# Kernel optimization log

Hardware: AMD Instinct MI355X
Metric: run time of the kernel (lower is better)

## Reference

```python
import jax, jax.numpy as jnp
import numpy as np

INNER = 256   # inner_channel
NODES = 64    # nodes_num (prototypes)
EM_NUM = 3
DIAG_C = 128  # hardcoded diag_channel in FullyConnectGCLayer


def setup_inputs() -> dict:
    key = jax.random.key(0)
    ks = jax.random.split(key, 16)
    b, c, w, h = 4, 1024, 64, 64
    f32 = jnp.float32
    d = {}
    d["x"] = jax.random.normal(ks[0], (b, c, w, h), f32)
    # Conv2d weights re-initialized to N(0, 0.001) in Intra_graph.__init__
    d["W_in"] = 0.001 * jax.random.normal(ks[1], (INNER, c), f32)
    d["b_in"] = jnp.zeros((INNER,), f32)
    d["multi_proto"] = 0.001 * jax.random.normal(ks[2], (1, INNER, NODES), f32)
    d["pi0"] = jnp.ones((1, NODES), f32) / NODES
    # Conv1d layers keep default kaiming-uniform-ish init
    lim = 1.0 / np.sqrt(INNER)
    d["W_adj"] = jax.random.uniform(ks[3], (DIAG_C, INNER), f32, -lim, lim)
    d["b_adj"] = jax.random.uniform(ks[4], (DIAG_C,), f32, -lim, lim)
    d["W_diag"] = jax.random.uniform(ks[5], (DIAG_C, INNER), f32, -lim, lim)
    d["b_diag"] = jax.random.uniform(ks[6], (DIAG_C,), f32, -lim, lim)
    d["gcn_weight"] = 0.01 * jax.random.normal(ks[7], (INNER, INNER), f32)
    d["W_out"] = 0.001 * jax.random.normal(ks[8], (c, INNER), f32)
    d["b_out"] = jnp.zeros((c,), f32)
    d["gamma"] = jnp.ones((c,), f32)
    d["beta"] = jnp.zeros((c,), f32)
    d["W_out2"] = 0.001 * jax.random.normal(ks[9], (c, INNER), f32)
    d["b_out2"] = jnp.zeros((c,), f32)
    d["gamma2"] = jnp.ones((c,), f32)
    d["beta2"] = jnp.zeros((c,), f32)
    d["flag"] = 0
    return d


def _bn(y, g, bt):
    # BatchNorm2d in training mode: batch stats over (N,H,W), biased var, eps=1e-5
    m = jnp.mean(y, (0, 2, 3), keepdims=True)
    v = jnp.var(y, (0, 2, 3), keepdims=True)
    return (y - m) * jax.lax.rsqrt(v + 1e-5) * g[None, :, None, None] + bt[None, :, None, None]


def _forward(x, W_in, b_in, multi_proto, pi0, W_adj, b_adj, W_diag, b_diag,
             gcn_weight, W_out, b_out, gamma, beta, W_out2, b_out2, gamma2, beta2):
    b, c, w, h = x.shape
    wh = w * h
    x1 = (jnp.einsum('oi,bihw->bohw', W_in, x) + b_in[None, :, None, None]).reshape(b, INNER, wh)
    # ---- EM soft-clustering loop (runs under no_grad in torch) ----
    x1s = jax.lax.stop_gradient(x1)
    mu = jnp.broadcast_to(multi_proto, (b, INNER, NODES))
    pi = jnp.broadcast_to(pi0[None, :, :], (b, 1, NODES))
    for _ in range(EM_NUM):
        lik = jnp.einsum('bcm,bcn->bmn', x1s, mu)              # [b, wh, n]
        lik = jnp.exp(lik - jnp.max(lik, 2, keepdims=True))
        post = lik * pi
        post = post / (1e-18 + jnp.sum(post, 2, keepdims=True))
        prob = post / (1e-18 + jnp.sum(post, 1, keepdims=True))
        mu = jnp.einsum('bcm,bmn->bcn', x1s, prob)
        pi = jnp.sum(post, 1, keepdims=True) / wh
    post = jax.lax.stop_gradient(post)
    prob = jax.lax.stop_gradient(prob)
    # ---- aggregate to prototypes (grad flows through x1 only) ----
    x2 = jnp.einsum('bcm,bmn->bcn', x1, prob)                   # [b, inner, n]
    # ---- branch 2: scatter back, conv, bn ----
    x4 = jnp.einsum('bcn,bmn->bcm', x2, post).reshape(b, INNER, w, h)
    x4 = _bn(jnp.einsum('oi,bihw->bohw', W_out2, x4) + b_out2[None, :, None, None], gamma2, beta2)
    output2 = jax.nn.relu(jax.nn.relu(x4) + x)
    # ---- FullyConnectGCLayer on x2 ----
    xd = jnp.einsum('oi,bin->bon', W_diag, x2) + b_diag[None, :, None]
    dvec = jax.nn.sigmoid(jnp.mean(xd, 2))                      # [b, 128]
    xa = jnp.einsum('oi,bin->bon', W_adj, x2) + b_adj[None, :, None]  # [b, 128, n]
    # sigmoid(diag(d)) has 0.5 off-diagonal, sigmoid(d) on diagonal:
    # xa^T S xa = 0.5 * (1^T xa)^T (1^T xa) + xa^T diag(sig(d)-0.5) xa
    u = jnp.sum(xa, 1)                                          # [b, n]
    A = 0.5 * u[:, :, None] * u[:, None, :] + jnp.einsum('bcn,bc,bcm->bnm', xa, dvec - 0.5, xa)
    A = jax.nn.relu(A) + jnp.eye(NODES, dtype=x.dtype)[None]
    deg = jax.lax.stop_gradient(jnp.sum(A, 1) ** -0.5)          # no_grad degree, [b, n]
    A = deg[:, :, None] * A * deg[:, None, :]
    gout = jnp.einsum('oi,bin->bon', gcn_weight, jnp.einsum('bcn,bnm->bcm', x2, A))
    x2g = jax.nn.relu(gout) + x2                                # res_connect
    # ---- branch 1: scatter back, conv, bn ----
    x3 = jnp.einsum('bcn,bmn->bcm', x2g, post).reshape(b, INNER, w, h)
    x3 = _bn(jnp.einsum('oi,bihw->bohw', W_out, x3) + b_out[None, :, None, None], gamma, beta)
    output = jax.nn.relu(jax.nn.relu(x3) + x)
    return output, output2


def reference(x, W_in, b_in, multi_proto, pi0, W_adj, b_adj, W_diag, b_diag,
              gcn_weight, W_out, b_out, gamma, beta, W_out2, b_out2, gamma2, beta2, flag):
    # flag only gates a buffer EMA update (no effect on forward outputs)
    return _forward(x, W_in, b_in, multi_proto, pi0, W_adj, b_adj, W_diag, b_diag,
                    gcn_weight, W_out, b_out, gamma, beta, W_out2, b_out2, gamma2, beta2)
```

## Files before the change

### kernel.cpp

```cpp
#include <hip/hip_runtime.h>
#include <math.h>


typedef unsigned short u16;
typedef short s16x8 __attribute__((ext_vector_type(8)));
typedef float f32x4 __attribute__((ext_vector_type(4)));

constexpr int BB  = 4;
constexpr int CH  = 1024;
constexpr int IN  = 256;
constexpr int ND  = 64;
constexpr int WH  = 4096;
constexpr int DCN = 128;
constexpr size_t TOT = (size_t)BB * CH * WH;

__device__ inline u16 f2bf(float f) {
  unsigned u = __float_as_uint(f);
  return (u16)((u + 0x7fffu + ((u >> 16) & 1u)) >> 16);
}
__device__ inline s16x8 ld8(const u16* p) { return *(const s16x8*)p; }
#define MFMA16(a, b, c) __builtin_amdgcn_mfma_f32_16x16x32_bf16(a, b, c, 0, 0, 0)

__global__ void k_init(const float* __restrict__ Win, const float* __restrict__ mp,
                       const float* __restrict__ pi0, u16* __restrict__ Winb,
                       u16* __restrict__ mu_t, float* __restrict__ piw,
                       float* __restrict__ sp) {
  int idx = blockIdx.x * 256 + threadIdx.x;
  if (idx < IN * CH) { Winb[idx] = f2bf(Win[idx]); return; }
  int j = idx - IN * CH;
  if (j < BB * ND * IN) {
    int bb = j >> 14, n = (j >> 8) & 63, c = j & 255;
    mu_t[((size_t)(bb * ND + n)) * IN + c] = f2bf(mp[c * ND + n]);
    return;
  }
  j -= BB * ND * IN;
  if (j < BB * ND) { piw[j] = pi0[j & 63]; return; }
  j -= BB * ND;
  if (j < 3 * BB * ND) sp[j] = 0.f;
}

__global__ __launch_bounds__(512) void k_x1(
    const float* __restrict__ x, const u16* __restrict__ Winb,
    const float* __restrict__ bin, u16* __restrict__ x1, u16* __restrict__ x1t) {
  __shared__ u16 lt[64][40];
  const int t = threadIdx.x, w = t >> 6, lr = t & 15, lg = (t >> 4) & 3;
  const int wc = w & 3, wm = w >> 2;
  const int m0 = blockIdx.x * 64, b = blockIdx.y;
  const int si = t >> 4, sm = (t & 15) * 4;
  const float* xb = x + (size_t)b * CH * WH + m0 + sm;
  f32x4 acc[4][2];
#pragma unroll
  for (int i = 0; i < 4; ++i)
#pragma unroll
    for (int j = 0; j < 2; ++j) acc[i][j] = (f32x4){0.f, 0.f, 0.f, 0.f};
  const u16* wp = Winb + (size_t)(wc * 64 + lr) * CH + lg * 8;

  float4 nxt = *(const float4*)&xb[(size_t)si * WH];
  for (int k0 = 0; k0 < CH; k0 += 32) {
    float4 cur = nxt;
    __syncthreads();
    lt[sm + 0][si] = f2bf(cur.x); lt[sm + 1][si] = f2bf(cur.y);
    lt[sm + 2][si] = f2bf(cur.z); lt[sm + 3][si] = f2bf(cur.w);
    if (k0 + 32 < CH) nxt = *(const float4*)&xb[(size_t)(k0 + 32 + si) * WH];
    __syncthreads();
    s16x8 af[4], bf[2];
#pragma unroll
    for (int i = 0; i < 4; ++i) af[i] = ld8(wp + (size_t)i * 16 * CH + k0);
#pragma unroll
    for (int j = 0; j < 2; ++j) bf[j] = *(const s16x8*)&lt[wm * 32 + j * 16 + lr][lg * 8];
#pragma unroll
    for (int i = 0; i < 4; ++i)
#pragma unroll
      for (int j = 0; j < 2; ++j) acc[i][j] = MFMA16(af[i], bf[j], acc[i][j]);
  }
#pragma unroll
  for (int i = 0; i < 4; ++i) {
    const int cb = wc * 64 + i * 16 + lg * 4;
    const float4 bi = *(const float4*)&bin[cb];
    const float bia[4] = {bi.x, bi.y, bi.z, bi.w};
#pragma unroll
    for (int j = 0; j < 2; ++j) {
      const int m = m0 + wm * 32 + j * 16 + lr;
      float v[4];
#pragma unroll
      for (int r = 0; r < 4; ++r) v[r] = acc[i][j][r] + bia[r];
      ushort4 o;
      o.x = f2bf(v[0]); o.y = f2bf(v[1]); o.z = f2bf(v[2]); o.w = f2bf(v[3]);
      *(ushort4*)&x1t[((size_t)b * WH + m) * IN + cb] = o;
#pragma unroll
      for (int r = 0; r < 4; ++r)
        x1[((size_t)b * IN + cb + r) * WH + m] = f2bf(v[r]);
    }
  }
}

__global__ __launch_bounds__(256) void k_em(
    const u16* __restrict__ x1, const u16* __restrict__ x1t,
    const u16* __restrict__ mu_t, const float* __restrict__ piw,
    float* __restrict__ sp, u16* __restrict__ pmn,
    float* __restrict__ mup, float* __restrict__ gp, int doG) {
  __shared__ u16 ptl[64][72];
  const int t = threadIdx.x, w = t >> 6, lr = t & 15, lg = (t >> 4) & 3;
  const int mch = blockIdx.x, b = blockIdx.y;
  {
    f32x4 acc[4];
#pragma unroll
    for (int f = 0; f < 4; ++f) acc[f] = (f32x4){0.f, 0.f, 0.f, 0.f};
    const u16* ap = x1t + ((size_t)b * WH + mch * 64 + w * 16 + lr) * IN + lg * 8;
    const u16* bp = mu_t + ((size_t)b * ND + lr) * IN + lg * 8;
#pragma unroll
    for (int k0 = 0; k0 < IN; k0 += 32) {
      s16x8 a = ld8(ap + k0);
#pragma unroll
      for (int f = 0; f < 4; ++f)
        acc[f] = MFMA16(a, ld8(bp + f * 16 * IN + k0), acc[f]);
    }
    float pi_[4], spart[4] = {0.f, 0.f, 0.f, 0.f};
#pragma unroll
    for (int f = 0; f < 4; ++f) pi_[f] = piw[b * ND + f * 16 + lr];
#pragma unroll
    for (int r = 0; r < 4; ++r) {
      float v0 = acc[0][r], v1 = acc[1][r], v2 = acc[2][r], v3 = acc[3][r];
      float mx = fmaxf(fmaxf(v0, v1), fmaxf(v2, v3));
      mx = fmaxf(mx, __shfl_xor(mx, 1)); mx = fmaxf(mx, __shfl_xor(mx, 2));
      mx = fmaxf(mx, __shfl_xor(mx, 4)); mx = fmaxf(mx, __shfl_xor(mx, 8));
      float e0 = __expf(v0 - mx) * pi_[0], e1 = __expf(v1 - mx) * pi_[1];
      float e2 = __expf(v2 - mx) * pi_[2], e3 = __expf(v3 - mx) * pi_[3];
      float s = e0 + e1 + e2 + e3;
      s += __shfl_xor(s, 1); s += __shfl_xor(s, 2);
      s += __shfl_xor(s, 4); s += __shfl_xor(s, 8);
      const float inv = 1.f / (1e-18f + s);
      e0 *= inv; e1 *= inv; e2 *= inv; e3 *= inv;
      const int mloc = w * 16 + lg * 4 + r;
      const size_t gbase = ((size_t)b * WH + mch * 64 + mloc) * ND + lr;
      u16 q0 = f2bf(e0), q1 = f2bf(e1), q2 = f2bf(e2), q3 = f2bf(e3);
      pmn[gbase + 0]  = q0; pmn[gbase + 16] = q1;
      pmn[gbase + 32] = q2; pmn[gbase + 48] = q3;
      ptl[0 + lr][mloc]  = q0; ptl[16 + lr][mloc] = q1;
      ptl[32 + lr][mloc] = q2; ptl[48 + lr][mloc] = q3;
      spart[0] += e0; spart[1] += e1; spart[2] += e2; spart[3] += e3;
    }
#pragma unroll
    for (int f = 0; f < 4; ++f) {
      spart[f] += __shfl_xor(spart[f], 16);
      spart[f] += __shfl_xor(spart[f], 32);
    }
    if (((t >> 4) & 3) == 0) {
#pragma unroll
      for (int f = 0; f < 4; ++f)
        atomicAdd(&sp[b * ND + f * 16 + lr], spart[f]);
    }
  }
  __syncthreads();
  {
    f32x4 acc[4][4];
#pragma unroll
    for (int i = 0; i < 4; ++i)
#pragma unroll
      for (int j = 0; j < 4; ++j) acc[i][j] = (f32x4){0.f, 0.f, 0.f, 0.f};
    const u16* ap = x1 + ((size_t)b * IN + w * 64 + lr) * WH + mch * 64 + lg * 8;
#pragma unroll
    for (int ks = 0; ks < 2; ++ks) {
      s16x8 af[4], bf[4];
#pragma unroll
      for (int i = 0; i < 4; ++i) af[i] = ld8(ap + (size_t)i * 16 * WH + ks * 32);
#pragma unroll
      for (int j = 0; j < 4; ++j)
        bf[j] = *(const s16x8*)&ptl[j * 16 + lr][ks * 32 + lg * 8];
#pragma unroll
      for (int i = 0; i < 4; ++i)
#pragma unroll
        for (int j = 0; j < 4; ++j) acc[i][j] = MFMA16(af[i], bf[j], acc[i][j]);
    }
    float* mo = mup + ((size_t)mch * BB + b) * (IN * ND);
#pragma unroll
    for (int i = 0; i < 4; ++i)
#pragma unroll
      for (int j = 0; j < 4; ++j)
#pragma unroll
        for (int r = 0; r < 4; ++r) {
          const int c = w * 64 + i * 16 + lg * 4 + r, n = j * 16 + lr;
          mo[c * ND + n] = acc[i][j][r];
        }
  }
  if (doG) {
    f32x4 acc[4];
#pragma unroll
    for (int j = 0; j < 4; ++j) acc[j] = (f32x4){0.f, 0.f, 0.f, 0.f};
#pragma unroll
    for (int ks = 0; ks < 2; ++ks) {
      s16x8 a = *(const s16x8*)&ptl[w * 16 + lr][ks * 32 + lg * 8];
#pragma unroll
      for (int j = 0; j < 4; ++j) {
        s16x8 bq = *(const s16x8*)&ptl[j * 16 + lr][ks * 32 + lg * 8];
        acc[j] = MFMA16(a, bq, acc[j]);
      }
    }
    float* go = gp + ((size_t)mch * BB + b) * (ND * ND);
#pragma unroll
    for (int j = 0; j < 4; ++j)
#pragma unroll
      for (int r = 0; r < 4; ++r) {
        const int n1 = w * 16 + lg * 4 + r, n2 = j * 16 + lr;
        go[n1 * ND + n2] = acc[j][r];
      }
  }
}

__global__ void k_mu_red(const float* __restrict__ mup, const float* __restrict__ spb,
                         float* __restrict__ piw, float* __restrict__ mu,
                         u16* __restrict__ mu_t, const float* __restrict__ gp,
                         float* __restrict__ G, int doG) {
  const int idx = blockIdx.x * 256 + threadIdx.x;
  const int bb = idx >> 14, c = (idx >> 6) & 255, n = idx & 63;
  float s = 0.f;
#pragma unroll 8
  for (int ch = 0; ch < 64; ++ch)
    s += mup[((size_t)ch * BB + bb) * (IN * ND) + (idx & 16383)];
  const float v = s / (1e-18f + spb[bb * ND + n]);
  mu[idx] = v;
  mu_t[((size_t)(bb * ND + n)) * IN + c] = f2bf(v);
  if (idx < BB * ND) piw[idx] = spb[idx] * (1.f / (float)WH);
  if (doG && idx < BB * ND * ND) {
    float g = 0.f;
#pragma unroll 8
    for (int ch = 0; ch < 64; ++ch) g += gp[(size_t)ch * (BB * ND * ND) + idx];
    G[idx] = g;
  }
}

__global__ __launch_bounds__(256) void k_gcA(
    const float* __restrict__ mu, const float* __restrict__ gw,
    const float* __restrict__ Wa, const float* __restrict__ ba,
    const float* __restrict__ Wd, const float* __restrict__ bd,
    float* __restrict__ qbuf, float* __restrict__ xabuf, float* __restrict__ dv) {
  __shared__ float sx2[IN * ND];
  __shared__ float srm[IN];
  const int t = threadIdx.x, blk = blockIdx.x, b = blockIdx.y;
  if (blk < 6) {
    const float* src = mu + (size_t)b * IN * ND;
#pragma unroll
    for (int q4 = 0; q4 < 16; ++q4)
      *(float4*)&sx2[q4 * 1024 + t * 4] = *(const float4*)&src[q4 * 1024 + t * 4];
    __syncthreads();
    const int rg = t >> 4, cg = t & 15;
    const float* W = (blk < 4) ? gw + (size_t)(blk * 64 + rg * 4) * IN
                               : Wa + (size_t)((blk - 4) * 64 + rg * 4) * IN;
    float acc[4][4] = {};
    for (int i4 = 0; i4 < 64; ++i4) {
      float4 xv[4];
#pragma unroll
      for (int e = 0; e < 4; ++e)
        xv[e] = *(const float4*)&sx2[(i4 * 4 + e) * 64 + cg * 4];
#pragma unroll
      for (int rr = 0; rr < 4; ++rr) {
        const float4 w4 = *(const float4*)&W[(size_t)rr * IN + i4 * 4];
        acc[rr][0] += w4.x * xv[0].x + w4.y * xv[1].x + w4.z * xv[2].x + w4.w * xv[3].x;
        acc[rr][1] += w4.x * xv[0].y + w4.y * xv[1].y + w4.z * xv[2].y + w4.w * xv[3].y;
        acc[rr][2] += w4.x * xv[0].z + w4.y * xv[1].z + w4.z * xv[2].z + w4.w * xv[3].z;
        acc[rr][3] += w4.x * xv[0].w + w4.y * xv[1].w + w4.z * xv[2].w + w4.w * xv[3].w;
      }
    }
    if (blk < 4) {
      float* dst = qbuf + (size_t)b * IN * ND + (size_t)(blk * 64 + rg * 4) * ND + cg * 4;
#pragma unroll
      for (int rr = 0; rr < 4; ++rr)
        *(float4*)&dst[(size_t)rr * ND] =
            make_float4(acc[rr][0], acc[rr][1], acc[rr][2], acc[rr][3]);
    } else {
      const int xr = (blk - 4) * 64 + rg * 4;
      float* dst = xabuf + (size_t)b * DCN * ND + (size_t)xr * ND + cg * 4;
#pragma unroll
      for (int rr = 0; rr < 4; ++rr) {
        const float bv = ba[xr + rr];
        *(float4*)&dst[(size_t)rr * ND] =
            make_float4(acc[rr][0] + bv, acc[rr][1] + bv, acc[rr][2] + bv, acc[rr][3] + bv);
      }
    }
  } else {
    {
      const float* row = mu + (size_t)b * IN * ND + (size_t)t * ND;
      float s = 0.f;
#pragma unroll
      for (int n4 = 0; n4 < 16; ++n4) {
        float4 v = *(const float4*)&row[n4 * 4];
        s += v.x + v.y + v.z + v.w;
      }
      srm[t] = s * (1.f / ND);
    }
    __syncthreads();
    if (t < DCN) {
      float a = 0.f;
#pragma unroll
      for (int i4 = 0; i4 < 64; ++i4) {
        float4 w4 = *(const float4*)&Wd[(size_t)t * IN + i4 * 4];
        float4 r4 = *(const float4*)&srm[i4 * 4];
        a += w4.x * r4.x + w4.y * r4.y + w4.z * r4.z + w4.w * r4.w;
      }
      a += bd[t];
      dv[b * DCN + t] = 1.f / (1.f + __expf(-a)) - 0.5f;
    }
  }
}

__global__ __launch_bounds__(256) void k_gcB(
    const float* __restrict__ xabuf, const float* __restrict__ dv,
    float* __restrict__ ahat) {
  __shared__ float sxa[DCN * ND];
  __shared__ float sdv[DCN];
  __shared__ float su[ND];
  __shared__ float sdeg[ND];
  __shared__ float sA[ND * 65];
  const int t = threadIdx.x, b = blockIdx.x;
  const float* src = xabuf + (size_t)b * DCN * ND;
#pragma unroll
  for (int q4 = 0; q4 < 8; ++q4)
    *(float4*)&sxa[q4 * 1024 + t * 4] = *(const float4*)&src[q4 * 1024 + t * 4];
  if (t < DCN) sdv[t] = dv[b * DCN + t];
  __syncthreads();
  if (t < ND) {
    float s = 0.f;
    for (int dc = 0; dc < DCN; ++dc) s += sxa[dc * ND + t];
    su[t] = s;
  }
  __syncthreads();
  {
    const int n1g = t >> 4, n2g = t & 15;
    float acc[4][4] = {};
    for (int dc = 0; dc < DCN; ++dc) {
      const float dvv = sdv[dc];
      float4 v1 = *(const float4*)&sxa[dc * ND + n1g * 4];
      const float4 v2 = *(const float4*)&sxa[dc * ND + n2g * 4];
      v1.x *= dvv; v1.y *= dvv; v1.z *= dvv; v1.w *= dvv;
      acc[0][0] += v1.x * v2.x; acc[0][1] += v1.x * v2.y;
      acc[0][2] += v1.x * v2.z; acc[0][3] += v1.x * v2.w;
      acc[1][0] += v1.y * v2.x; acc[1][1] += v1.y * v2.y;
      acc[1][2] += v1.y * v2.z; acc[1][3] += v1.y * v2.w;
      acc[2][0] += v1.z * v2.x; acc[2][1] += v1.z * v2.y;
      acc[2][2] += v1.z * v2.z; acc[2][3] += v1.z * v2.w;
      acc[3][0] += v1.w * v2.x; acc[3][1] += v1.w * v2.y;
      acc[3][2] += v1.w * v2.z; acc[3][3] += v1.w * v2.w;
    }
#pragma unroll
    for (int i = 0; i < 4; ++i) {
      const int n1 = n1g * 4 + i;
      const float u1 = su[n1];
#pragma unroll
      for (int j = 0; j < 4; ++j) {
        const int n2 = n2g * 4 + j;
        const float v = acc[i][j] + 0.5f * u1 * su[n2];
        sA[n1 * 65 + n2] = fmaxf(v, 0.f) + (n1 == n2 ? 1.f : 0.f);
      }
    }
  }
  __syncthreads();
  if (t < ND) {
    float s = 0.f;
    for (int m = 0; m < ND; ++m) s += sA[m * 65 + t];
    sdeg[t] = rsqrtf(s);
  }
  __syncthreads();
  {
    const int n1g = t >> 4, n2g = t & 15;
#pragma unroll
    for (int i = 0; i < 4; ++i) {
      const int n1 = n1g * 4 + i;
      const float dr = sdeg[n1];
      float4 o;
      o.x = dr * sA[n1 * 65 + n2g * 4 + 0] * sdeg[n2g * 4 + 0];
      o.y = dr * sA[n1 * 65 + n2g * 4 + 1] * sdeg[n2g * 4 + 1];
      o.z = dr * sA[n1 * 65 + n2g * 4 + 2] * sdeg[n2g * 4 + 2];
      o.w = dr * sA[n1 * 65 + n2g * 4 + 3] * sdeg[n2g * 4 + 3];
      *(float4*)&ahat[(size_t)b * ND * ND + n1 * ND + n2g * 4] = o;
    }
  }
}

__global__ __launch_bounds__(256) void k_gcC(
    const float* __restrict__ qbuf, const float* __restrict__ ahat,
    const float* __restrict__ mu, float* __restrict__ x2g) {
  __shared__ float sq[64 * 68];
  __shared__ float sAh[64 * 65];
  const int t = threadIdx.x, ro = blockIdx.x * 64, b = blockIdx.y;
  {
    const int r = t >> 2, seg = (t & 3) * 16;
    const float* qs = qbuf + (size_t)b * IN * ND + (size_t)(ro + r) * ND + seg;
#pragma unroll
    for (int f = 0; f < 4; ++f) {
      float4 v = *(const float4*)&qs[f * 4];
      sq[r * 68 + seg + f * 4 + 0] = v.x; sq[r * 68 + seg + f * 4 + 1] = v.y;
      sq[r * 68 + seg + f * 4 + 2] = v.z; sq[r * 68 + seg + f * 4 + 3] = v.w;
    }
    const float* as = ahat + (size_t)b * ND * ND + (size_t)r * ND + seg;
#pragma unroll
    for (int f = 0; f < 4; ++f) {
      float4 v = *(const float4*)&as[f * 4];
      sAh[r * 65 + seg + f * 4 + 0] = v.x; sAh[r * 65 + seg + f * 4 + 1] = v.y;
      sAh[r * 65 + seg + f * 4 + 2] = v.z; sAh[r * 65 + seg + f * 4 + 3] = v.w;
    }
  }
  __syncthreads();
  const int rg = t >> 4, cg = t & 15;
  float acc[4][4] = {};
  for (int k = 0; k < ND; ++k) {
    const float4 a4 = *(const float4*)&sAh[k * 65 + cg * 4];
    float qv[4];
#pragma unroll
    for (int rr = 0; rr < 4; ++rr) qv[rr] = sq[(rg * 4 + rr) * 68 + k];
#pragma unroll
    for (int rr = 0; rr < 4; ++rr) {
      acc[rr][0] += qv[rr] * a4.x; acc[rr][1] += qv[rr] * a4.y;
      acc[rr][2] += qv[rr] * a4.z; acc[rr][3] += qv[rr] * a4.w;
    }
  }
#pragma unroll
  for (int rr = 0; rr < 4; ++rr) {
    const size_t off = (size_t)b * IN * ND + (size_t)(ro + rg * 4 + rr) * ND + cg * 4;
    const float4 xv = *(const float4*)&mu[off];
    float4 o;
    o.x = fmaxf(acc[rr][0], 0.f) + xv.x; o.y = fmaxf(acc[rr][1], 0.f) + xv.y;
    o.z = fmaxf(acc[rr][2], 0.f) + xv.z; o.w = fmaxf(acc[rr][3], 0.f) + xv.w;
    *(float4*)&x2g[off] = o;
  }
}

__global__ __launch_bounds__(256) void k_zdual(
    const float* __restrict__ Wo, const float* __restrict__ v1,
    float* __restrict__ z1o, u16* __restrict__ zb1o,
    const float* __restrict__ Wo2, const float* __restrict__ v2,
    float* __restrict__ z2o, u16* __restrict__ zb2o) {
  const float* W = blockIdx.z ? Wo2 : Wo;
  const float* v = blockIdx.z ? v2 : v1;
  float* z  = blockIdx.z ? z2o : z1o;
  u16* zb   = blockIdx.z ? zb2o : zb1o;
  __shared__ float As[16][68];
  __shared__ float Bs[16][64];
  const int t = threadIdx.x, tx = t & 15, ty = t >> 4;
  const int o0 = blockIdx.x * 64, bb = blockIdx.y;
  const int aoo = t >> 2, akq = (t & 3) * 4;
  const int bkk = t >> 4, bnq = (t & 15) * 4;
  float acc[4][4] = {};
  for (int k0 = 0; k0 < IN; k0 += 16) {
    {
      float4 w4 = *(const float4*)&W[(size_t)(o0 + aoo) * IN + k0 + akq];
      As[akq + 0][aoo] = w4.x; As[akq + 1][aoo] = w4.y;
      As[akq + 2][aoo] = w4.z; As[akq + 3][aoo] = w4.w;
    }
    *(float4*)&Bs[bkk][bnq] = *(const float4*)&v[((size_t)bb * IN + k0 + bkk) * ND + bnq];
    __syncthreads();
#pragma unroll
    for (int kk = 0; kk < 16; ++kk) {
      float4 a4 = *(const float4*)&As[kk][ty * 4];
      float4 b4 = *(const float4*)&Bs[kk][tx * 4];
      float ar[4] = {a4.x, a4.y, a4.z, a4.w}, br[4] = {b4.x, b4.y, b4.z, b4.w};
#pragma unroll
      for (int i = 0; i < 4; ++i)
#pragma unroll
        for (int j = 0; j < 4; ++j) acc[i][j] += ar[i] * br[j];
    }
    __syncthreads();
  }
#pragma unroll
  for (int i = 0; i < 4; ++i) {
    float4 r = make_float4(acc[i][0], acc[i][1], acc[i][2], acc[i][3]);
    const size_t off = ((size_t)bb * CH + o0 + ty * 4 + i) * ND + tx * 4;
    *(float4*)&z[off] = r;
    ushort4 h;
    h.x = f2bf(r.x); h.y = f2bf(r.y); h.z = f2bf(r.z); h.w = f2bf(r.w);
    *(ushort4*)&zb[off] = h;
  }
}

__global__ __launch_bounds__(256) void k_stats(
    const float* __restrict__ z1, const float* __restrict__ z2,
    const float* __restrict__ sp, const float* __restrict__ G,
    const float* __restrict__ gam, const float* __restrict__ bet,
    const float* __restrict__ gam2, const float* __restrict__ bet2,
    float* __restrict__ abc) {
  const int t = threadIdx.x;
  const int o = blockIdx.x * 4 + (t >> 6), lane = t & 63;
#pragma unroll
  for (int br = 0; br < 2; ++br) {
    const float* z = br ? z2 : z1;
    float macc = 0.f, eacc = 0.f;
    for (int bb = 0; bb < BB; ++bb) {
      const float zv = z[((size_t)bb * CH + o) * ND + lane];
      float s1 = zv * sp[bb * ND + lane];
      const float* Gb = G + (size_t)bb * ND * ND;
      float gz = 0.f;
      for (int k = 0; k < ND; ++k) {
        const float zk = __shfl(zv, k);
        gz += Gb[k * ND + lane] * zk;
      }
      float q = zv * gz;
#pragma unroll
      for (int off = 32; off; off >>= 1) {
        s1 += __shfl_xor(s1, off);
        q  += __shfl_xor(q, off);
      }
      macc += s1; eacc += q;
    }
    const float inv = 1.f / (float)((size_t)BB * WH);
    const float mean = macc * inv;
    const float var  = eacc * inv - mean * mean;
    const float a = (br ? gam2[o] : gam[o]) * rsqrtf(var + 1e-5f);
    const float c = (br ? bet2[o] : bet[o]) - mean * a;
    if (lane == 0) { abc[br * 2 * CH + o] = a; abc[br * 2 * CH + CH + o] = c; }
  }
}

__global__ __launch_bounds__(256) void k_epi(
    const u16* __restrict__ zb1, const u16* __restrict__ zb2,
    const u16* __restrict__ post, const float* __restrict__ abc,
    const float* __restrict__ x, float* __restrict__ out1, float* __restrict__ out2) {
  const int t = threadIdx.x, w = t >> 6, lr = t & 15, lg = (t >> 4) & 3;
  const int m0 = blockIdx.x * 256 + w * 64, o0 = blockIdx.y * 64, bb = blockIdx.z;
  f32x4 acc1[4][4], acc2[4][4];
#pragma unroll
  for (int i = 0; i < 4; ++i)
#pragma unroll
    for (int j = 0; j < 4; ++j) {
      acc1[i][j] = (f32x4){0.f, 0.f, 0.f, 0.f};
      acc2[i][j] = (f32x4){0.f, 0.f, 0.f, 0.f};
    }
  const u16* z1p = zb1 + ((size_t)bb * CH + o0 + lr) * ND + lg * 8;
  const u16* z2p = zb2 + ((size_t)bb * CH + o0 + lr) * ND + lg * 8;
  const u16* pp  = post + ((size_t)bb * WH + m0 + lr) * ND + lg * 8;
#pragma unroll
  for (int ks = 0; ks < 2; ++ks) {
    s16x8 a1[4], a2[4], bq[4];
#pragma unroll
    for (int i = 0; i < 4; ++i) {
      a1[i] = ld8(z1p + i * 16 * ND + ks * 32);
      a2[i] = ld8(z2p + i * 16 * ND + ks * 32);
    }
#pragma unroll
    for (int j = 0; j < 4; ++j) bq[j] = ld8(pp + j * 16 * ND + ks * 32);
#pragma unroll
    for (int i = 0; i < 4; ++i)
#pragma unroll
      for (int j = 0; j < 4; ++j) {
        acc1[i][j] = MFMA16(a1[i], bq[j], acc1[i][j]);
        acc2[i][j] = MFMA16(a2[i], bq[j], acc2[i][j]);
      }
  }
#pragma unroll
  for (int i = 0; i < 4; ++i)
#pragma unroll
    for (int r = 0; r < 4; ++r) {
      const int o = o0 + i * 16 + lg * 4 + r;
      const float a1v = abc[o], c1v = abc[CH + o];
      const float a2v = abc[2 * CH + o], c2v = abc[3 * CH + o];
      const size_t base = ((size_t)bb * CH + o) * WH + m0 + lr;
#pragma unroll
      for (int j = 0; j < 4; ++j) {
        const size_t off = base + j * 16;
        const float xv = x[off];
        out1[off] = fmaxf(fmaxf(a1v * acc1[i][j][r] + c1v, 0.f) + xv, 0.f);
        out2[off] = fmaxf(fmaxf(a2v * acc2[i][j][r] + c2v, 0.f) + xv, 0.f);
      }
    }
}

extern "C" void kernel_launch(void* const* d_in, const int* in_sizes, int n_in,
                              void* d_out, int out_size, void* d_ws, size_t ws_size,
                              hipStream_t stream) {
  (void)in_sizes; (void)n_in; (void)out_size; (void)ws_size;
  const float* x    = (const float*)d_in[0];
  const float* Win  = (const float*)d_in[1];
  const float* bin  = (const float*)d_in[2];
  const float* mp   = (const float*)d_in[3];
  const float* pi0  = (const float*)d_in[4];
  const float* Wa   = (const float*)d_in[5];
  const float* ba   = (const float*)d_in[6];
  const float* Wd   = (const float*)d_in[7];
  const float* bd   = (const float*)d_in[8];
  const float* gw   = (const float*)d_in[9];
  const float* Wo   = (const float*)d_in[10];
  const float* gam  = (const float*)d_in[12];
  const float* bet  = (const float*)d_in[13];
  const float* Wo2  = (const float*)d_in[14];
  const float* gam2 = (const float*)d_in[16];
  const float* bet2 = (const float*)d_in[17];

  char* ob = (char*)d_out;
  char* wp = (char*)d_ws;
  float* mup = (float*)(ob + 0);
  float* gp  = (float*)(ob + 16777216);
  float* z1  = (float*)(ob + 20971520);
  float* z2  = (float*)(ob + 22020096);
  u16*   x1    = (u16*)(wp + 0);
  u16*   x1t   = (u16*)(wp + 8388608);
  u16*   Winb  = (u16*)(wp + 16777216);
  u16*   mu_t  = (u16*)(wp + 17301504);
  u16*   pmn   = (u16*)(wp + 17432576);
  float* mu    = (float*)(wp + 19529728);
  float* x2g   = (float*)(wp + 19791872);
  u16*   zb1   = (u16*)(wp + 20054016);
  u16*   zb2   = (u16*)(wp + 20578304);
  float* sp3   = (float*)(wp + 21102592);
  float* piw   = (float*)(wp + 21105664);
  float* abc   = (float*)(wp + 21106688);
  float* G     = (float*)(wp + 21123072);
  float* qbuf  = (float*)(wp + 21188608);
  float* xabuf = (float*)(wp + 21450752);
  float* dvb   = (float*)(wp + 21581824);
  float* ahat  = (float*)(wp + 21583872);
  float* out1  = (float*)d_out;
  float* out2  = out1 + TOT;

  k_init<<<dim3(1284), 256, 0, stream>>>(Win, mp, pi0, Winb, mu_t, piw, sp3);
  k_x1<<<dim3(64, BB), 512, 0, stream>>>(x, Winb, bin, x1, x1t);
  for (int it = 0; it < 3; ++it) {
    float* spb = sp3 + it * 256;
    const int doG = (it == 2);
    k_em<<<dim3(64, BB), 256, 0, stream>>>(x1, x1t, mu_t, piw, spb, pmn, mup, gp, doG);
    k_mu_red<<<dim3(256), 256, 0, stream>>>(mup, spb, piw, mu, mu_t, gp, G, doG);
  }
  k_gcA<<<dim3(7, BB), 256, 0, stream>>>(mu, gw, Wa, ba, Wd, bd, qbuf, xabuf, dvb);
  k_gcB<<<dim3(BB), 256, 0, stream>>>(xabuf, dvb, ahat);
  k_gcC<<<dim3(4, BB), 256, 0, stream>>>(qbuf, ahat, mu, x2g);
  k_zdual<<<dim3(16, BB, 2), 256, 0, stream>>>(Wo, x2g, z1, zb1, Wo2, mu, z2, zb2);
  k_stats<<<dim3(256), 256, 0, stream>>>(z1, z2, sp3 + 512, G, gam, bet, gam2, bet2, abc);
  k_epi<<<dim3(16, 16, BB), 256, 0, stream>>>(zb1, zb2, pmn, abc, x, out1, out2);
}
```

Before: 232.9 us.

## Enlarge EM tiles, skip redundant pmn writes, fuse GCN and z2 kernels

The EM kernel now covers 256 spatial positions per block instead of 64. This cuts the partial-mu buffer and its reduction from 64 chunks to 16, and the posterior matrix is written to global memory only on the last iteration. The z2 projection runs concurrently inside the gcA kernel, and gcB and gcC are merged so the normalized adjacency stays in shared memory. The epilogue uses nontemporal loads and stores. In exchange, the EM grid drops to 64 blocks, which may underfill the GPU, and the fused kernel uses large shared memory.

```diff
diff --git a/kernel.cpp b/kernel.cpp
--- a/kernel.cpp
+++ b/kernel.cpp
@@ -98,48 +98,60 @@
     const u16* __restrict__ x1, const u16* __restrict__ x1t,
     const u16* __restrict__ mu_t, const float* __restrict__ piw,
     float* __restrict__ sp, u16* __restrict__ pmn,
-    float* __restrict__ mup, float* __restrict__ gp, int doG) {
-  __shared__ u16 ptl[64][72];
+    float* __restrict__ mup, float* __restrict__ gp, int doLast) {
+  __shared__ u16 ptl[64][264];
   const int t = threadIdx.x, w = t >> 6, lr = t & 15, lg = (t >> 4) & 3;
   const int mch = blockIdx.x, b = blockIdx.y;
+  const int mbase = mch * 256;
   {
-    f32x4 acc[4];
-#pragma unroll
-    for (int f = 0; f < 4; ++f) acc[f] = (f32x4){0.f, 0.f, 0.f, 0.f};
-    const u16* ap = x1t + ((size_t)b * WH + mch * 64 + w * 16 + lr) * IN + lg * 8;
+    f32x4 acc[4][4];
+#pragma unroll
+    for (int i = 0; i < 4; ++i)
+#pragma unroll
+      for (int f = 0; f < 4; ++f) acc[i][f] = (f32x4){0.f, 0.f, 0.f, 0.f};
+    const u16* ap = x1t + ((size_t)b * WH + mbase + w * 64 + lr) * IN + lg * 8;
     const u16* bp = mu_t + ((size_t)b * ND + lr) * IN + lg * 8;
 #pragma unroll
     for (int k0 = 0; k0 < IN; k0 += 32) {
-      s16x8 a = ld8(ap + k0);
-#pragma unroll
-      for (int f = 0; f < 4; ++f)
-        acc[f] = MFMA16(a, ld8(bp + f * 16 * IN + k0), acc[f]);
+      s16x8 bf[4];
+#pragma unroll
+      for (int f = 0; f < 4; ++f) bf[f] = ld8(bp + f * 16 * IN + k0);
+#pragma unroll
+      for (int i = 0; i < 4; ++i) {
+        s16x8 av = ld8(ap + (size_t)i * 16 * IN + k0);
+#pragma unroll
+        for (int f = 0; f < 4; ++f) acc[i][f] = MFMA16(av, bf[f], acc[i][f]);
+      }
     }
     float pi_[4], spart[4] = {0.f, 0.f, 0.f, 0.f};
 #pragma unroll
     for (int f = 0; f < 4; ++f) pi_[f] = piw[b * ND + f * 16 + lr];
 #pragma unroll
-    for (int r = 0; r < 4; ++r) {
-      float v0 = acc[0][r], v1 = acc[1][r], v2 = acc[2][r], v3 = acc[3][r];
-      float mx = fmaxf(fmaxf(v0, v1), fmaxf(v2, v3));
-      mx = fmaxf(mx, __shfl_xor(mx, 1)); mx = fmaxf(mx, __shfl_xor(mx, 2));
-      mx = fmaxf(mx, __shfl_xor(mx, 4)); mx = fmaxf(mx, __shfl_xor(mx, 8));
-      float e0 = __expf(v0 - mx) * pi_[0], e1 = __expf(v1 - mx) * pi_[1];
-      float e2 = __expf(v2 - mx) * pi_[2], e3 = __expf(v3 - mx) * pi_[3];
-      float s = e0 + e1 + e2 + e3;
-      s += __shfl_xor(s, 1); s += __shfl_xor(s, 2);
-      s += __shfl_xor(s, 4); s += __shfl_xor(s, 8);
-      const float inv = 1.f / (1e-18f + s);
-      e0 *= inv; e1 *= inv; e2 *= inv; e3 *= inv;
-      const int mloc = w * 16 + lg * 4 + r;
-      const size_t gbase = ((size_t)b * WH + mch * 64 + mloc) * ND + lr;
-      u16 q0 = f2bf(e0), q1 = f2bf(e1), q2 = f2bf(e2), q3 = f2bf(e3);
-      pmn[gbase + 0]  = q0; pmn[gbase + 16] = q1;
-      pmn[gbase + 32] = q2; pmn[gbase + 48] = q3;
-      ptl[0 + lr][mloc]  = q0; ptl[16 + lr][mloc] = q1;
-      ptl[32 + lr][mloc] = q2; ptl[48 + lr][mloc] = q3;
-      spart[0] += e0; spart[1] += e1; spart[2] += e2; spart[3] += e3;
-    }
+    for (int i = 0; i < 4; ++i)
+#pragma unroll
+      for (int r = 0; r < 4; ++r) {
+        float v0 = acc[i][0][r], v1 = acc[i][1][r], v2 = acc[i][2][r], v3 = acc[i][3][r];
+        float mx = fmaxf(fmaxf(v0, v1), fmaxf(v2, v3));
+        mx = fmaxf(mx, __shfl_xor(mx, 1)); mx = fmaxf(mx, __shfl_xor(mx, 2));
+        mx = fmaxf(mx, __shfl_xor(mx, 4)); mx = fmaxf(mx, __shfl_xor(mx, 8));
+        float e0 = __expf(v0 - mx) * pi_[0], e1 = __expf(v1 - mx) * pi_[1];
+        float e2 = __expf(v2 - mx) * pi_[2], e3 = __expf(v3 - mx) * pi_[3];
+        float s = e0 + e1 + e2 + e3;
+        s += __shfl_xor(s, 1); s += __shfl_xor(s, 2);
+        s += __shfl_xor(s, 4); s += __shfl_xor(s, 8);
+        const float inv = 1.f / (1e-18f + s);
+        e0 *= inv; e1 *= inv; e2 *= inv; e3 *= inv;
+        const int mloc = w * 64 + i * 16 + lg * 4 + r;
+        u16 q0 = f2bf(e0), q1 = f2bf(e1), q2 = f2bf(e2), q3 = f2bf(e3);
+        ptl[0 + lr][mloc]  = q0; ptl[16 + lr][mloc] = q1;
+        ptl[32 + lr][mloc] = q2; ptl[48 + lr][mloc] = q3;
+        if (doLast) {
+          const size_t gbase = ((size_t)b * WH + mbase + mloc) * ND + lr;
+          pmn[gbase + 0]  = q0; pmn[gbase + 16] = q1;
+          pmn[gbase + 32] = q2; pmn[gbase + 48] = q3;
+        }
+        spart[0] += e0; spart[1] += e1; spart[2] += e2; spart[3] += e3;
+      }
 #pragma unroll
     for (int f = 0; f < 4; ++f) {
       spart[f] += __shfl_xor(spart[f], 16);
@@ -158,9 +170,9 @@
     for (int i = 0; i < 4; ++i)
 #pragma unroll
       for (int j = 0; j < 4; ++j) acc[i][j] = (f32x4){0.f, 0.f, 0.f, 0.f};
-    const u16* ap = x1 + ((size_t)b * IN + w * 64 + lr) * WH + mch * 64 + lg * 8;
-#pragma unroll
-    for (int ks = 0; ks < 2; ++ks) {
+    const u16* ap = x1 + ((size_t)b * IN + w * 64 + lr) * WH + mbase + lg * 8;
+#pragma unroll
+    for (int ks = 0; ks < 8; ++ks) {
       s16x8 af[4], bf[4];
 #pragma unroll
       for (int i = 0; i < 4; ++i) af[i] = ld8(ap + (size_t)i * 16 * WH + ks * 32);
@@ -183,17 +195,17 @@
           mo[c * ND + n] = acc[i][j][r];
         }
   }
-  if (doG) {
+  if (doLast) {
     f32x4 acc[4];
 #pragma unroll
     for (int j = 0; j < 4; ++j) acc[j] = (f32x4){0.f, 0.f, 0.f, 0.f};
 #pragma unroll
-    for (int ks = 0; ks < 2; ++ks) {
-      s16x8 a = *(const s16x8*)&ptl[w * 16 + lr][ks * 32 + lg * 8];
+    for (int ks = 0; ks < 8; ++ks) {
+      s16x8 av = *(const s16x8*)&ptl[w * 16 + lr][ks * 32 + lg * 8];
 #pragma unroll
       for (int j = 0; j < 4; ++j) {
         s16x8 bq = *(const s16x8*)&ptl[j * 16 + lr][ks * 32 + lg * 8];
-        acc[j] = MFMA16(a, bq, acc[j]);
+        acc[j] = MFMA16(av, bq, acc[j]);
       }
     }
     float* go = gp + ((size_t)mch * BB + b) * (ND * ND);
@@ -214,8 +226,8 @@
   const int idx = blockIdx.x * 256 + threadIdx.x;
   const int bb = idx >> 14, c = (idx >> 6) & 255, n = idx & 63;
   float s = 0.f;
-#pragma unroll 8
-  for (int ch = 0; ch < 64; ++ch)
+#pragma unroll
+  for (int ch = 0; ch < 16; ++ch)
     s += mup[((size_t)ch * BB + bb) * (IN * ND) + (idx & 16383)];
   const float v = s / (1e-18f + spb[bb * ND + n]);
   mu[idx] = v;
@@ -223,100 +235,160 @@
   if (idx < BB * ND) piw[idx] = spb[idx] * (1.f / (float)WH);
   if (doG && idx < BB * ND * ND) {
     float g = 0.f;
-#pragma unroll 8
-    for (int ch = 0; ch < 64; ++ch) g += gp[(size_t)ch * (BB * ND * ND) + idx];
+#pragma unroll
+    for (int ch = 0; ch < 16; ++ch) g += gp[(size_t)ch * (BB * ND * ND) + idx];
     G[idx] = g;
   }
 }
 
-__global__ __launch_bounds__(256) void k_gcA(
+__device__ void zg_body(const float* __restrict__ W, const float* __restrict__ v,
+                        float* __restrict__ z, u16* __restrict__ zb,
+                        int o0, int bb, int t, char* smem) {
+  float (*As)[68] = (float(*)[68])smem;
+  float (*Bs)[64] = (float(*)[64])(smem + 4352);
+  const int tx = t & 15, ty = t >> 4;
+  const int aoo = t >> 2, akq = (t & 3) * 4;
+  const int bkk = t >> 4, bnq = (t & 15) * 4;
+  float acc[4][4] = {};
+  for (int k0 = 0; k0 < IN; k0 += 16) {
+    {
+      float4 w4 = *(const float4*)&W[(size_t)(o0 + aoo) * IN + k0 + akq];
+      As[akq + 0][aoo] = w4.x; As[akq + 1][aoo] = w4.y;
+      As[akq + 2][aoo] = w4.z; As[akq + 3][aoo] = w4.w;
+    }
+    *(float4*)&Bs[bkk][bnq] = *(const float4*)&v[((size_t)bb * IN + k0 + bkk) * ND + bnq];
+    __syncthreads();
+#pragma unroll
+    for (int kk = 0; kk < 16; ++kk) {
+      float4 a4 = *(const float4*)&As[kk][ty * 4];
+      float4 b4 = *(const float4*)&Bs[kk][tx * 4];
+      float ar[4] = {a4.x, a4.y, a4.z, a4.w}, br[4] = {b4.x, b4.y, b4.z, b4.w};
+#pragma unroll
+      for (int i = 0; i < 4; ++i)
+#pragma unroll
+        for (int j = 0; j < 4; ++j) acc[i][j] += ar[i] * br[j];
+    }
+    __syncthreads();
+  }
+#pragma unroll
+  for (int i = 0; i < 4; ++i) {
+    float4 r = make_float4(acc[i][0], acc[i][1], acc[i][2], acc[i][3]);
+    const size_t off = ((size_t)bb * CH + o0 + ty * 4 + i) * ND + tx * 4;
+    *(float4*)&z[off] = r;
+    ushort4 h;
+    h.x = f2bf(r.x); h.y = f2bf(r.y); h.z = f2bf(r.z); h.w = f2bf(r.w);
+    *(ushort4*)&zb[off] = h;
+  }
+}
+
+__global__ __launch_bounds__(256) void k_gcAz2(
     const float* __restrict__ mu, const float* __restrict__ gw,
     const float* __restrict__ Wa, const float* __restrict__ ba,
     const float* __restrict__ Wd, const float* __restrict__ bd,
-    float* __restrict__ qbuf, float* __restrict__ xabuf, float* __restrict__ dv) {
-  __shared__ float sx2[IN * ND];
-  __shared__ float srm[IN];
-  const int t = threadIdx.x, blk = blockIdx.x, b = blockIdx.y;
-  if (blk < 6) {
-    const float* src = mu + (size_t)b * IN * ND;
-#pragma unroll
-    for (int q4 = 0; q4 < 16; ++q4)
-      *(float4*)&sx2[q4 * 1024 + t * 4] = *(const float4*)&src[q4 * 1024 + t * 4];
-    __syncthreads();
-    const int rg = t >> 4, cg = t & 15;
-    const float* W = (blk < 4) ? gw + (size_t)(blk * 64 + rg * 4) * IN
-                               : Wa + (size_t)((blk - 4) * 64 + rg * 4) * IN;
-    float acc[4][4] = {};
-    for (int i4 = 0; i4 < 64; ++i4) {
-      float4 xv[4];
-#pragma unroll
-      for (int e = 0; e < 4; ++e)
-        xv[e] = *(const float4*)&sx2[(i4 * 4 + e) * 64 + cg * 4];
-#pragma unroll
-      for (int rr = 0; rr < 4; ++rr) {
-        const float4 w4 = *(const float4*)&W[(size_t)rr * IN + i4 * 4];
-        acc[rr][0] += w4.x * xv[0].x + w4.y * xv[1].x + w4.z * xv[2].x + w4.w * xv[3].x;
-        acc[rr][1] += w4.x * xv[0].y + w4.y * xv[1].y + w4.z * xv[2].y + w4.w * xv[3].y;
-        acc[rr][2] += w4.x * xv[0].z + w4.y * xv[1].z + w4.z * xv[2].z + w4.w * xv[3].z;
-        acc[rr][3] += w4.x * xv[0].w + w4.y * xv[1].w + w4.z * xv[2].w + w4.w * xv[3].w;
-      }
-    }
-    if (blk < 4) {
-      float* dst = qbuf + (size_t)b * IN * ND + (size_t)(blk * 64 + rg * 4) * ND + cg * 4;
-#pragma unroll
-      for (int rr = 0; rr < 4; ++rr)
-        *(float4*)&dst[(size_t)rr * ND] =
-            make_float4(acc[rr][0], acc[rr][1], acc[rr][2], acc[rr][3]);
+    float* __restrict__ qbuf, float* __restrict__ xabuf, float* __restrict__ dv,
+    const float* __restrict__ Wo2, float* __restrict__ z2, u16* __restrict__ zb2) {
+  __shared__ __align__(16) char smem[66560];
+  const int t = threadIdx.x, bid = blockIdx.x;
+  if (bid < 28) {
+    const int blk = bid % 7, b = bid / 7;
+    float* sx2 = (float*)smem;
+    float* srm = (float*)(smem + 65536);
+    if (blk < 6) {
+      const float* src = mu + (size_t)b * IN * ND;
+#pragma unroll
+      for (int q4 = 0; q4 < 16; ++q4)
+        *(float4*)&sx2[q4 * 1024 + t * 4] = *(const float4*)&src[q4 * 1024 + t * 4];
+      __syncthreads();
+      const int rg = t >> 4, cg2 = t & 15;
+      const float* W = (blk < 4) ? gw + (size_t)(blk * 64 + rg * 4) * IN
+                                 : Wa + (size_t)((blk - 4) * 64 + rg * 4) * IN;
+      float acc[4][4] = {};
+      for (int i4 = 0; i4 < 64; ++i4) {
+        float4 xv[4];
+#pragma unroll
+        for (int e = 0; e < 4; ++e)
+          xv[e] = *(const float4*)&sx2[(i4 * 4 + e) * 64 + cg2 * 4];
+#pragma unroll
+        for (int rr = 0; rr < 4; ++rr) {
+          const float4 w4 = *(const float4*)&W[(size_t)rr * IN + i4 * 4];
+          acc[rr][0] += w4.x * xv[0].x + w4.y * xv[1].x + w4.z * xv[2].x + w4.w * xv[3].x;
+          acc[rr][1] += w4.x * xv[0].y + w4.y * xv[1].y + w4.z * xv[2].y + w4.w * xv[3].y;
+          acc[rr][2] += w4.x * xv[0].z + w4.y * xv[1].z + w4.z * xv[2].z + w4.w * xv[3].z;
+          acc[rr][3] += w4.x * xv[0].w + w4.y * xv[1].w + w4.z * xv[2].w + w4.w * xv[3].w;
+        }
+      }
+      if (blk < 4) {
+        float* dst = qbuf + (size_t)b * IN * ND + (size_t)(blk * 64 + rg * 4) * ND + cg2 * 4;
+#pragma unroll
+        for (int rr = 0; rr < 4; ++rr)
+          *(float4*)&dst[(size_t)rr * ND] =
+              make_float4(acc[rr][0], acc[rr][1], acc[rr][2], acc[rr][3]);
+      } else {
+        const int xr = (blk - 4) * 64 + rg * 4;
+        float* dst = xabuf + (size_t)b * DCN * ND + (size_t)xr * ND + cg2 * 4;
+#pragma unroll
+        for (int rr = 0; rr < 4; ++rr) {
+          const float bv = ba[xr + rr];
+          *(float4*)&dst[(size_t)rr * ND] =
+              make_float4(acc[rr][0] + bv, acc[rr][1] + bv, acc[rr][2] + bv, acc[rr][3] + bv);
+        }
+      }
     } else {
-      const int xr = (blk - 4) * 64 + rg * 4;
-      float* dst = xabuf + (size_t)b * DCN * ND + (size_t)xr * ND + cg * 4;
-#pragma unroll
-      for (int rr = 0; rr < 4; ++rr) {
-        const float bv = ba[xr + rr];
-        *(float4*)&dst[(size_t)rr * ND] =
-            make_float4(acc[rr][0] + bv, acc[rr][1] + bv, acc[rr][2] + bv, acc[rr][3] + bv);
-      }
-    }
-  } else {
-    {
-      const float* row = mu + (size_t)b * IN * ND + (size_t)t * ND;
-      float s = 0.f;
-#pragma unroll
-      for (int n4 = 0; n4 < 16; ++n4) {
-        float4 v = *(const float4*)&row[n4 * 4];
-        s += v.x + v.y + v.z + v.w;
-      }
-      srm[t] = s * (1.f / ND);
-    }
-    __syncthreads();
-    if (t < DCN) {
-      float a = 0.f;
-#pragma unroll
-      for (int i4 = 0; i4 < 64; ++i4) {
-        float4 w4 = *(const float4*)&Wd[(size_t)t * IN + i4 * 4];
-        float4 r4 = *(const float4*)&srm[i4 * 4];
-        a += w4.x * r4.x + w4.y * r4.y + w4.z * r4.z + w4.w * r4.w;
-      }
-      a += bd[t];
-      dv[b * DCN + t] = 1.f / (1.f + __expf(-a)) - 0.5f;
-    }
-  }
-}
-
-__global__ __launch_bounds__(256) void k_gcB(
+      {
+        const float* row = mu + (size_t)b * IN * ND + (size_t)t * ND;
+        float s = 0.f;
+#pragma unroll
+        for (int n4 = 0; n4 < 16; ++n4) {
+          float4 v = *(const float4*)&row[n4 * 4];
+          s += v.x + v.y + v.z + v.w;
+        }
+        srm[t] = s * (1.f / ND);
+      }
+      __syncthreads();
+      if (t < DCN) {
+        float av = 0.f;
+#pragma unroll
+        for (int i4 = 0; i4 < 64; ++i4) {
+          float4 w4 = *(const float4*)&Wd[(size_t)t * IN + i4 * 4];
+          float4 r4 = *(const float4*)&srm[i4 * 4];
+          av += w4.x * r4.x + w4.y * r4.y + w4.z * r4.z + w4.w * r4.w;
+        }
+        av += bd[t];
+        dv[b * DCN + t] = 1.f / (1.f + __expf(-av)) - 0.5f;
+      }
+    }
+  } else if (bid >= 32 && bid < 96) {
+    const int zid = bid - 32;
+    zg_body(Wo2, mu, z2, zb2, (zid & 15) * 64, zid >> 4, t, smem);
+  }
+}
+
+__global__ __launch_bounds__(256) void k_gcBC(
     const float* __restrict__ xabuf, const float* __restrict__ dv,
-    float* __restrict__ ahat) {
+    const float* __restrict__ qbuf, const float* __restrict__ mu,
+    float* __restrict__ x2g) {
   __shared__ float sxa[DCN * ND];
+  __shared__ float sA[ND * 65];
+  __shared__ float sq[64 * 68];
   __shared__ float sdv[DCN];
   __shared__ float su[ND];
   __shared__ float sdeg[ND];
-  __shared__ float sA[ND * 65];
-  const int t = threadIdx.x, b = blockIdx.x;
-  const float* src = xabuf + (size_t)b * DCN * ND;
-#pragma unroll
-  for (int q4 = 0; q4 < 8; ++q4)
-    *(float4*)&sxa[q4 * 1024 + t * 4] = *(const float4*)&src[q4 * 1024 + t * 4];
-  if (t < DCN) sdv[t] = dv[b * DCN + t];
+  const int t = threadIdx.x, qtr = blockIdx.x, b = blockIdx.y;
+  {
+    const float* src = xabuf + (size_t)b * DCN * ND;
+#pragma unroll
+    for (int q4 = 0; q4 < 8; ++q4)
+      *(float4*)&sxa[q4 * 1024 + t * 4] = *(const float4*)&src[q4 * 1024 + t * 4];
+    if (t < DCN) sdv[t] = dv[b * DCN + t];
+    const int r = t >> 2, seg = (t & 3) * 16;
+    const float* qs = qbuf + (size_t)b * IN * ND + (size_t)(qtr * 64 + r) * ND + seg;
+#pragma unroll
+    for (int f = 0; f < 4; ++f) {
+      float4 v = *(const float4*)&qs[f * 4];
+      sq[r * 68 + seg + f * 4 + 0] = v.x; sq[r * 68 + seg + f * 4 + 1] = v.y;
+      sq[r * 68 + seg + f * 4 + 2] = v.z; sq[r * 68 + seg + f * 4 + 3] = v.w;
+    }
+  }
   __syncthreads();
   if (t < ND) {
     float s = 0.f;
@@ -366,109 +438,43 @@
     for (int i = 0; i < 4; ++i) {
       const int n1 = n1g * 4 + i;
       const float dr = sdeg[n1];
+#pragma unroll
+      for (int e = 0; e < 4; ++e)
+        sA[n1 * 65 + n2g * 4 + e] *= dr * sdeg[n2g * 4 + e];
+    }
+  }
+  __syncthreads();
+  {
+    const int rg = t >> 4, cg2 = t & 15;
+    float acc[4][4] = {};
+    for (int k = 0; k < ND; ++k) {
+      const float4 a4 = *(const float4*)&sA[k * 65 + cg2 * 4];
+      float qv[4];
+#pragma unroll
+      for (int rr = 0; rr < 4; ++rr) qv[rr] = sq[(rg * 4 + rr) * 68 + k];
+#pragma unroll
+      for (int rr = 0; rr < 4; ++rr) {
+        acc[rr][0] += qv[rr] * a4.x; acc[rr][1] += qv[rr] * a4.y;
+        acc[rr][2] += qv[rr] * a4.z; acc[rr][3] += qv[rr] * a4.w;
+      }
+    }
+#pragma unroll
+    for (int rr = 0; rr < 4; ++rr) {
+      const size_t off = (size_t)b * IN * ND + (size_t)(qtr * 64 + rg * 4 + rr) * ND + cg2 * 4;
+      const float4 xv = *(const float4*)&mu[off];
       float4 o;
-      o.x = dr * sA[n1 * 65 + n2g * 4 + 0] * sdeg[n2g * 4 + 0];
-      o.y = dr * sA[n1 * 65 + n2g * 4 + 1] * sdeg[n2g * 4 + 1];
-      o.z = dr * sA[n1 * 65 + n2g * 4 + 2] * sdeg[n2g * 4 + 2];
-      o.w = dr * sA[n1 * 65 + n2g * 4 + 3] * sdeg[n2g * 4 + 3];
-      *(float4*)&ahat[(size_t)b * ND * ND + n1 * ND + n2g * 4] = o;
-    }
-  }
-}
-
-__global__ __launch_bounds__(256) void k_gcC(
-    const float* __restrict__ qbuf, const float* __restrict__ ahat,
-    const float* __restrict__ mu, float* __restrict__ x2g) {
-  __shared__ float sq[64 * 68];
-  __shared__ float sAh[64 * 65];
-  const int t = threadIdx.x, ro = blockIdx.x * 64, b = blockIdx.y;
-  {
-    const int r = t >> 2, seg = (t & 3) * 16;
-    const float* qs = qbuf + (size_t)b * IN * ND + (size_t)(ro + r) * ND + seg;
-#pragma unroll
-    for (int f = 0; f < 4; ++f) {
-      float4 v = *(const float4*)&qs[f * 4];
-      sq[r * 68 + seg + f * 4 + 0] = v.x; sq[r * 68 + seg + f * 4 + 1] = v.y;
-      sq[r * 68 + seg + f * 4 + 2] = v.z; sq[r * 68 + seg + f * 4 + 3] = v.w;
-    }
-    const float* as = ahat + (size_t)b * ND * ND + (size_t)r * ND + seg;
-#pragma unroll
-    for (int f = 0; f < 4; ++f) {
-      float4 v = *(const float4*)&as[f * 4];
-      sAh[r * 65 + seg + f * 4 + 0] = v.x; sAh[r * 65 + seg + f * 4 + 1] = v.y;
-      sAh[r * 65 + seg + f * 4 + 2] = v.z; sAh[r * 65 + seg + f * 4 + 3] = v.w;
-    }
-  }
-  __syncthreads();
-  const int rg = t >> 4, cg = t & 15;
-  float acc[4][4] = {};
-  for (int k = 0; k < ND; ++k) {
-    const float4 a4 = *(const float4*)&sAh[k * 65 + cg * 4];
-    float qv[4];
-#pragma unroll
-    for (int rr = 0; rr < 4; ++rr) qv[rr] = sq[(rg * 4 + rr) * 68 + k];
-#pragma unroll
-    for (int rr = 0; rr < 4; ++rr) {
-      acc[rr][0] += qv[rr] * a4.x; acc[rr][1] += qv[rr] * a4.y;
-      acc[rr][2] += qv[rr] * a4.z; acc[rr][3] += qv[rr] * a4.w;
-    }
-  }
-#pragma unroll
-  for (int rr = 0; rr < 4; ++rr) {
-    const size_t off = (size_t)b * IN * ND + (size_t)(ro + rg * 4 + rr) * ND + cg * 4;
-    const float4 xv = *(const float4*)&mu[off];
-    float4 o;
-    o.x = fmaxf(acc[rr][0], 0.f) + xv.x; o.y = fmaxf(acc[rr][1], 0.f) + xv.y;
-    o.z = fmaxf(acc[rr][2], 0.f) + xv.z; o.w = fmaxf(acc[rr][3], 0.f) + xv.w;
-    *(float4*)&x2g[off] = o;
-  }
-}
-
-__global__ __launch_bounds__(256) void k_zdual(
-    const float* __restrict__ Wo, const float* __restrict__ v1,
-    float* __restrict__ z1o, u16* __restrict__ zb1o,
-    const float* __restrict__ Wo2, const float* __restrict__ v2,
-    float* __restrict__ z2o, u16* __restrict__ zb2o) {
-  const float* W = blockIdx.z ? Wo2 : Wo;
-  const float* v = blockIdx.z ? v2 : v1;
-  float* z  = blockIdx.z ? z2o : z1o;
-  u16* zb   = blockIdx.z ? zb2o : zb1o;
-  __shared__ float As[16][68];
-  __shared__ float Bs[16][64];
-  const int t = threadIdx.x, tx = t & 15, ty = t >> 4;
-  const int o0 = blockIdx.x * 64, bb = blockIdx.y;
-  const int aoo = t >> 2, akq = (t & 3) * 4;
-  const int bkk = t >> 4, bnq = (t & 15) * 4;
-  float acc[4][4] = {};
-  for (int k0 = 0; k0 < IN; k0 += 16) {
-    {
-      float4 w4 = *(const float4*)&W[(size_t)(o0 + aoo) * IN + k0 + akq];
-      As[akq + 0][aoo] = w4.x; As[akq + 1][aoo] = w4.y;
-      As[akq + 2][aoo] = w4.z; As[akq + 3][aoo] = w4.w;
-    }
-    *(float4*)&Bs[bkk][bnq] = *(const float4*)&v[((size_t)bb * IN + k0 + bkk) * ND + bnq];
-    __syncthreads();
-#pragma unroll
-    for (int kk = 0; kk < 16; ++kk) {
-      float4 a4 = *(const float4*)&As[kk][ty * 4];
-      float4 b4 = *(const float4*)&Bs[kk][tx * 4];
-      float ar[4] = {a4.x, a4.y, a4.z, a4.w}, br[4] = {b4.x, b4.y, b4.z, b4.w};
-#pragma unroll
-      for (int i = 0; i < 4; ++i)
-#pragma unroll
-        for (int j = 0; j < 4; ++j) acc[i][j] += ar[i] * br[j];
-    }
-    __syncthreads();
-  }
-#pragma unroll
-  for (int i = 0; i < 4; ++i) {
-    float4 r = make_float4(acc[i][0], acc[i][1], acc[i][2], acc[i][3]);
-    const size_t off = ((size_t)bb * CH + o0 + ty * 4 + i) * ND + tx * 4;
-    *(float4*)&z[off] = r;
-    ushort4 h;
-    h.x = f2bf(r.x); h.y = f2bf(r.y); h.z = f2bf(r.z); h.w = f2bf(r.w);
-    *(ushort4*)&zb[off] = h;
-  }
+      o.x = fmaxf(acc[rr][0], 0.f) + xv.x; o.y = fmaxf(acc[rr][1], 0.f) + xv.y;
+      o.z = fmaxf(acc[rr][2], 0.f) + xv.z; o.w = fmaxf(acc[rr][3], 0.f) + xv.w;
+      *(float4*)&x2g[off] = o;
+    }
+  }
+}
+
+__global__ __launch_bounds__(256) void k_zg(
+    const float* __restrict__ W, const float* __restrict__ v,
+    float* __restrict__ z, u16* __restrict__ zb) {
+  __shared__ __align__(16) char smem[8448];
+  zg_body(W, v, z, zb, blockIdx.x * 64, blockIdx.y, threadIdx.x, smem);
 }
 
 __global__ __launch_bounds__(256) void k_stats(
@@ -555,9 +561,11 @@
 #pragma unroll
       for (int j = 0; j < 4; ++j) {
         const size_t off = base + j * 16;
-        const float xv = x[off];
-        out1[off] = fmaxf(fmaxf(a1v * acc1[i][j][r] + c1v, 0.f) + xv, 0.f);
-        out2[off] = fmaxf(fmaxf(a2v * acc2[i][j][r] + c2v, 0.f) + xv, 0.f);
+        const float xv = __builtin_nontemporal_load(&x[off]);
+        const float r1 = fmaxf(fmaxf(a1v * acc1[i][j][r] + c1v, 0.f) + xv, 0.f);
+        const float r2 = fmaxf(fmaxf(a2v * acc2[i][j][r] + c2v, 0.f) + xv, 0.f);
+        __builtin_nontemporal_store(r1, &out1[off]);
+        __builtin_nontemporal_store(r2, &out2[off]);
       }
     }
 }
@@ -586,9 +594,9 @@
   char* ob = (char*)d_out;
   char* wp = (char*)d_ws;
   float* mup = (float*)(ob + 0);
-  float* gp  = (float*)(ob + 16777216);
-  float* z1  = (float*)(ob + 20971520);
-  float* z2  = (float*)(ob + 22020096);
+  float* gp  = (float*)(ob + 4194304);
+  float* z1  = (float*)(ob + 5242880);
+  float* z2  = (float*)(ob + 6291456);
   u16*   x1    = (u16*)(wp + 0);
   u16*   x1t   = (u16*)(wp + 8388608);
   u16*   Winb  = (u16*)(wp + 16777216);
@@ -605,7 +613,6 @@
   float* qbuf  = (float*)(wp + 21188608);
   float* xabuf = (float*)(wp + 21450752);
   float* dvb   = (float*)(wp + 21581824);
-  float* ahat  = (float*)(wp + 21583872);
   float* out1  = (float*)d_out;
   float* out2  = out1 + TOT;
 
@@ -613,14 +620,14 @@
   k_x1<<<dim3(64, BB), 512, 0, stream>>>(x, Winb, bin, x1, x1t);
   for (int it = 0; it < 3; ++it) {
     float* spb = sp3 + it * 256;
-    const int doG = (it == 2);
-    k_em<<<dim3(64, BB), 256, 0, stream>>>(x1, x1t, mu_t, piw, spb, pmn, mup, gp, doG);
-    k_mu_red<<<dim3(256), 256, 0, stream>>>(mup, spb, piw, mu, mu_t, gp, G, doG);
-  }
-  k_gcA<<<dim3(7, BB), 256, 0, stream>>>(mu, gw, Wa, ba, Wd, bd, qbuf, xabuf, dvb);
-  k_gcB<<<dim3(BB), 256, 0, stream>>>(xabuf, dvb, ahat);
-  k_gcC<<<dim3(4, BB), 256, 0, stream>>>(qbuf, ahat, mu, x2g);
-  k_zdual<<<dim3(16, BB, 2), 256, 0, stream>>>(Wo, x2g, z1, zb1, Wo2, mu, z2, zb2);
+    const int doLast = (it == 2);
+    k_em<<<dim3(16, BB), 256, 0, stream>>>(x1, x1t, mu_t, piw, spb, pmn, mup, gp, doLast);
+    k_mu_red<<<dim3(256), 256, 0, stream>>>(mup, spb, piw, mu, mu_t, gp, G, doLast);
+  }
+  k_gcAz2<<<dim3(96), 256, 0, stream>>>(mu, gw, Wa, ba, Wd, bd, qbuf, xabuf, dvb,
+                                        Wo2, z2, zb2);
+  k_gcBC<<<dim3(4, BB), 256, 0, stream>>>(xabuf, dvb, qbuf, mu, x2g);
+  k_zg<<<dim3(16, BB), 256, 0, stream>>>(Wo, x2g, z1, zb1);
   k_stats<<<dim3(256), 256, 0, stream>>>(z1, z2, sp3 + 512, G, gam, bet, gam2, bet2, abc);
   k_epi<<<dim3(16, 16, BB), 256, 0, stream>>>(zb1, zb2, pmn, abc, x, out1, out2);
 }
```

After: 276.5 us. 1.19x slower.
